# Kernel optimization log

Hardware: AMD Instinct MI355X
Metric: run time of the kernel (lower is better)

Reference implementation:

```python
import jax, jax.numpy as jnp
import numpy as np

N, E, C, D, H = 50000, 1600000, 50000, 128, 512


def setup_inputs() -> dict:
    key = jax.random.key(0)
    ks = jax.random.split(key, 16)
    s = jnp.float32(0.02)  # keep activations stable through 3 layers
    inp = {}
    inp["x"] = jax.random.normal(ks[0], (N, D), jnp.float32)
    inp["edge_index"] = jax.random.randint(ks[1], (2, E), 0, N)
    inp["first_edge"] = jax.random.randint(ks[2], (2,), 0, N)
    inp["candidate_edges"] = jax.random.randint(ks[3], (C, 2), 0, N)
    inp["t"] = jax.random.uniform(ks[4], (1, 1), jnp.float32)
    dims = [(D, H), (H, H), (H, H)]
    i = 5
    for l, (di, do) in enumerate(dims):
        inp[f"gin{l}_w1"] = jax.random.normal(ks[i], (di, do), jnp.float32) * s; i += 1
        inp[f"gin{l}_b1"] = jnp.zeros((do,), jnp.float32)
        inp[f"gin{l}_w2"] = jax.random.normal(ks[i], (do, do), jnp.float32) * s; i += 1
        inp[f"gin{l}_b2"] = jnp.zeros((do,), jnp.float32)
    inp["pred_w1"] = jax.random.normal(ks[i], (5 * H, H), jnp.float32) * s; i += 1
    inp["pred_b1"] = jnp.zeros((H,), jnp.float32)
    inp["pred_w2"] = jax.random.normal(ks[i], (H, 1), jnp.float32) * s; i += 1
    inp["pred_b2"] = jnp.zeros((1,), jnp.float32)
    inp["time_w1"] = jax.random.normal(ks[i], (1, H), jnp.float32) * s; i += 1
    inp["time_b1"] = jnp.zeros((H,), jnp.float32)
    inp["time_w2"] = jax.random.normal(ks[i], (H, H), jnp.float32) * s; i += 1
    inp["time_b2"] = jnp.zeros((H,), jnp.float32)
    return inp


def _edge_rep(x, u, v):
    # 'sum_absdiff': cat([x_u + x_v, |x_u - x_v|]) -> 2*H features
    xu, xv = x[u], x[v]
    return jnp.concatenate([xu + xv, jnp.abs(xu - xv)], axis=-1)


def reference(x, edge_index, first_edge, candidate_edges, t,
              gin0_w1, gin0_b1, gin0_w2, gin0_b2,
              gin1_w1, gin1_b1, gin1_w2, gin1_b2,
              gin2_w1, gin2_b1, gin2_w2, gin2_b2,
              pred_w1, pred_b1, pred_w2, pred_b2,
              time_w1, time_b1, time_w2, time_b2):
    src, dst = edge_index[0], edge_index[1]
    layers = [(gin0_w1, gin0_b1, gin0_w2, gin0_b2),
              (gin1_w1, gin1_b1, gin1_w2, gin1_b2),
              (gin2_w1, gin2_b1, gin2_w2, gin2_b2)]
    # GINConv (eps=0): h_i = MLP(x_i + sum_{j->i} x_j)
    for w1, b1, w2, b2 in layers:
        agg = jax.ops.segment_sum(x[src], dst, num_segments=x.shape[0])
        h = x + agg
        x = jax.nn.relu(h @ w1 + b1) @ w2 + b2
    first_feat = _edge_rep(x, first_edge[0], first_edge[1])  # [2H]
    t_embed = (jax.nn.relu(t @ time_w1 + time_b1) @ time_w2 + time_b2)[0]  # [H]
    cand_feat = _edge_rep(x, candidate_edges[:, 0], candidate_edges[:, 1])  # [C, 2H]
    Cn = cand_feat.shape[0]
    feat = jnp.concatenate([
        jnp.broadcast_to(first_feat, (Cn, first_feat.shape[0])),
        cand_feat,
        jnp.broadcast_to(t_embed, (Cn, t_embed.shape[0])),
    ], axis=-1)  # [C, 5H]
    logits = (jax.nn.relu(feat @ pred_w1 + pred_b1) @ pred_w2 + pred_b2)[:, 0]  # [C]
    return logits
```

## Files before the change

kernel.cpp:

```cpp
#include <hip/hip_runtime.h>

typedef __bf16 bf16x2 __attribute__((ext_vector_type(2)));
typedef __bf16 bf16x4 __attribute__((ext_vector_type(4)));
typedef __bf16 bf16x8 __attribute__((ext_vector_type(8)));
typedef float f32x4 __attribute__((ext_vector_type(4)));

#define LDSTR 40

__global__ void hist_kernel(const int* __restrict__ dst, int* __restrict__ deg, int E) {
    int i = blockIdx.x * 256 + threadIdx.x;
    if (i < E) atomicAdd(&deg[dst[i]], 1);
}

__global__ __launch_bounds__(1024)
void scan_kernel(const int* __restrict__ deg, int* __restrict__ rowptr,
                 int* __restrict__ cursor, int n) {
    __shared__ int part[1024];
    int tid = threadIdx.x;
    int chunk = (n + 1023) >> 10;
    int beg = tid * chunk;
    int fin = min(beg + chunk, n);
    int s = 0;
    for (int i = beg; i < fin; i++) s += deg[i];
    part[tid] = s;
    __syncthreads();
    for (int off = 1; off < 1024; off <<= 1) {
        int v = (tid >= off) ? part[tid - off] : 0;
        __syncthreads();
        part[tid] += v;
        __syncthreads();
    }
    int run = (tid == 0) ? 0 : part[tid - 1];
    for (int i = beg; i < fin; i++) {
        rowptr[i] = run; cursor[i] = run; run += deg[i];
    }
    if (tid == 1023) rowptr[n] = run;
}

__global__ void scatter_kernel(const int* __restrict__ src, const int* __restrict__ dst,
                               int* __restrict__ cursor, int* __restrict__ colsrc, int E) {
    int i = blockIdx.x * 256 + threadIdx.x;
    if (i < E) {
        int p = atomicAdd(&cursor[dst[i]], 1);
        colsrc[p] = src[i];
    }
}

__global__ void f32_to_bf16_kernel(const float* __restrict__ in, __bf16* __restrict__ out, int n4) {
    int i = blockIdx.x * 256 + threadIdx.x;
    if (i < n4) {
        float4 f = ((const float4*)in)[i];
        bf16x4 o;
        o[0] = (__bf16)f.x; o[1] = (__bf16)f.y; o[2] = (__bf16)f.z; o[3] = (__bf16)f.w;
        ((bf16x4*)out)[i] = o;
    }
}

__global__ void wprep_kernel(const float* __restrict__ in, __bf16* __restrict__ out, int kbits) {
    int idx = blockIdx.x * 256 + threadIdx.x;
    int K = 1 << kbits;
    if (idx < (512 << kbits)) {
        int k = idx & (K - 1);
        int n = idx >> kbits;
        out[idx] = (__bf16)in[k * 512 + n];
    }
}

template<int F> struct VecT;
template<> struct VecT<2> { using T = bf16x2; };
template<> struct VecT<8> { using T = bf16x8; };

template<int F, int U>
__global__ __launch_bounds__(256)
void agg_kernel(const __bf16* __restrict__ xb, const int* __restrict__ rowptr,
                const int* __restrict__ colsrc, __bf16* __restrict__ h, int n) {
    const int node = blockIdx.x * 4 + (threadIdx.x >> 6);
    if (node >= n) return;
    const int lane = threadIdx.x & 63;
    const int DIM = F * 64;
    using V = typename VecT<F>::T;

    float acc[F];
    {
        V v = *(const V*)(xb + (size_t)node * DIM + lane * F);
        #pragma unroll
        for (int i = 0; i < F; i++) acc[i] = (float)v[i];
    }

    int e   = __builtin_amdgcn_readfirstlane(rowptr[node]);
    int end = __builtin_amdgcn_readfirstlane(rowptr[node + 1]);
    const __bf16* xl = xb + lane * F;

    for (; e + U <= end; e += U) {
        int s[U];
        #pragma unroll
        for (int j = 0; j < U; j++) s[j] = colsrc[e + j];
        V v[U];
        #pragma unroll
        for (int j = 0; j < U; j++) v[j] = *(const V*)(xl + (size_t)s[j] * DIM);
        #pragma unroll
        for (int j = 0; j < U; j++)
            #pragma unroll
            for (int i = 0; i < F; i++) acc[i] += (float)v[j][i];
    }
    if constexpr (U > 4) {
        for (; e + 4 <= end; e += 4) {
            int s[4];
            #pragma unroll
            for (int j = 0; j < 4; j++) s[j] = colsrc[e + j];
            V v[4];
            #pragma unroll
            for (int j = 0; j < 4; j++) v[j] = *(const V*)(xl + (size_t)s[j] * DIM);
            #pragma unroll
            for (int j = 0; j < 4; j++)
                #pragma unroll
                for (int i = 0; i < F; i++) acc[i] += (float)v[j][i];
        }
    }
    for (; e < end; e++) {
        int s0 = colsrc[e];
        V v = *(const V*)(xl + (size_t)s0 * DIM);
        #pragma unroll
        for (int i = 0; i < F; i++) acc[i] += (float)v[i];
    }

    __bf16* out = h + (size_t)node * DIM + lane * F;
    V o;
    #pragma unroll
    for (int i = 0; i < F; i++) o[i] = (__bf16)acc[i];
    *(V*)out = o;
}

template<int AMODE, bool RELU>
__global__ __launch_bounds__(256, 3)
void gemm_kernel(const __bf16* __restrict__ A, const __bf16* __restrict__ Xb,
                 const int* __restrict__ cand, const __bf16* __restrict__ Bt,
                 const float* __restrict__ bias, __bf16* __restrict__ Cout,
                 int M, int K) {
    __shared__ __bf16 sA[64 * LDSTR];
    __shared__ __bf16 sB[256 * LDSTR];

    const int tid = threadIdx.x;
    const int lane = tid & 63;
    const int waveN = tid >> 6;
    const int mlane = lane & 15;
    const int quad = lane >> 4;
    const int rowBase = blockIdx.x * 64;
    const int nBase = blockIdx.y * 256;

    const int ar = tid >> 2;
    const int ac = (tid & 3) << 3;
    const int br = tid >> 2;
    const int bc = (tid & 3) << 3;

    const f32x4 fzero = {0.f, 0.f, 0.f, 0.f};
    f32x4 acc[4][4];
    #pragma unroll
    for (int i = 0; i < 4; i++)
        #pragma unroll
        for (int j = 0; j < 4; j++) acc[i][j] = fzero;

    int uu = 0, vv = 0;
    const int grow = rowBase + ar;
    if (AMODE == 1 && grow < M) { uu = cand[2 * grow]; vv = cand[2 * grow + 1]; }

    for (int k0 = 0; k0 < K; k0 += 32) {
        __syncthreads();
        {
            bf16x8 av = {};
            if (AMODE == 0) {
                if (grow < M) av = *(const bf16x8*)(A + (size_t)grow * K + k0 + ac);
            } else {
                if (grow < M) {
                    int k = k0 + ac;
                    int kk = k & 511;
                    bf16x8 xu = *(const bf16x8*)(Xb + (size_t)uu * 512 + kk);
                    bf16x8 xv = *(const bf16x8*)(Xb + (size_t)vv * 512 + kk);
                    if (k < 512) {
                        #pragma unroll
                        for (int q = 0; q < 8; q++) av[q] = (__bf16)((float)xu[q] + (float)xv[q]);
                    } else {
                        #pragma unroll
                        for (int q = 0; q < 8; q++) av[q] = (__bf16)fabsf((float)xu[q] - (float)xv[q]);
                    }
                }
            }
            *(bf16x8*)(sA + ar * LDSTR + ac) = av;
        }
        #pragma unroll
        for (int i = 0; i < 4; i++) {
            int nn = br + i * 64;
            bf16x8 b = *(const bf16x8*)(Bt + (size_t)(nBase + nn) * K + k0 + bc);
            *(bf16x8*)(sB + nn * LDSTR + bc) = b;
        }
        __syncthreads();

        bf16x8 aF[4], bF[4];
        #pragma unroll
        for (int mt = 0; mt < 4; mt++)
            aF[mt] = *(const bf16x8*)(sA + (mt * 16 + mlane) * LDSTR + quad * 8);
        #pragma unroll
        for (int nt = 0; nt < 4; nt++)
            bF[nt] = *(const bf16x8*)(sB + (waveN * 64 + nt * 16 + mlane) * LDSTR + quad * 8);
        #pragma unroll
        for (int mt = 0; mt < 4; mt++)
            #pragma unroll
            for (int nt = 0; nt < 4; nt++)
                acc[mt][nt] = __builtin_amdgcn_mfma_f32_16x16x32_bf16(aF[mt], bF[nt], acc[mt][nt], 0, 0, 0);
    }

    #pragma unroll
    for (int mt = 0; mt < 4; mt++) {
        #pragma unroll
        for (int nt = 0; nt < 4; nt++) {
            int col = nBase + waveN * 64 + nt * 16 + mlane;
            float bv = bias[col];
            #pragma unroll
            for (int r = 0; r < 4; r++) {
                int row = rowBase + mt * 16 + quad * 4 + r;
                if (row < M) {
                    float v = acc[mt][nt][r] + bv;
                    if (RELU) v = fmaxf(v, 0.f);
                    Cout[(size_t)row * 512 + col] = (__bf16)v;
                }
            }
        }
    }
}

__global__ __launch_bounds__(512)
void constvec_kernel(const __bf16* __restrict__ xb, const int* __restrict__ first_edge,
                     const float* __restrict__ t,
                     const float* __restrict__ tw1, const float* __restrict__ tb1,
                     const float* __restrict__ tw2, const float* __restrict__ tb2,
                     const float* __restrict__ pw1, const float* __restrict__ pb1,
                     float* __restrict__ cvec) {
    __shared__ float z1[512];
    __shared__ float te[512];
    __shared__ float ff[1024];
    int tid = threadIdx.x;
    float tv = t[0];
    z1[tid] = fmaxf(tv * tw1[tid] + tb1[tid], 0.f);
    int u = first_edge[0], v = first_edge[1];
    float xu = (float)xb[(size_t)u * 512 + tid];
    float xv = (float)xb[(size_t)v * 512 + tid];
    ff[tid] = xu + xv;
    ff[512 + tid] = fabsf(xu - xv);
    __syncthreads();
    float s = tb2[tid];
    for (int j = 0; j < 512; j++) s += z1[j] * tw2[j * 512 + tid];
    te[tid] = s;
    __syncthreads();
    float c = pb1[tid];
    for (int k = 0; k < 1024; k++) c += ff[k] * pw1[k * 512 + tid];
    for (int j = 0; j < 512; j++) c += te[j] * pw1[(2048 + j) * 512 + tid];
    cvec[tid] = c;
}

__global__ __launch_bounds__(256)
void logits_kernel(const __bf16* __restrict__ Z, const float* __restrict__ w2,
                   const float* __restrict__ b2, float* __restrict__ out, int C) {
    int c = blockIdx.x * 4 + (threadIdx.x >> 6);
    if (c >= C) return;
    int lane = threadIdx.x & 63;
    bf16x8 z = *(const bf16x8*)(Z + (size_t)c * 512 + lane * 8);
    const float4* w = (const float4*)(w2 + lane * 8);
    float4 w0 = w[0], w1 = w[1];
    float s = (float)z[0] * w0.x + (float)z[1] * w0.y + (float)z[2] * w0.z + (float)z[3] * w0.w
            + (float)z[4] * w1.x + (float)z[5] * w1.y + (float)z[6] * w1.z + (float)z[7] * w1.w;
    #pragma unroll
    for (int off = 32; off > 0; off >>= 1) s += __shfl_down(s, off);
    if (lane == 0) out[c] = s + b2[0];
}

extern "C" void kernel_launch(void* const* d_in, const int* in_sizes, int n_in,
                              void* d_out, int out_size, void* d_ws, size_t ws_size,
                              hipStream_t stream) {
    (void)n_in; (void)out_size; (void)ws_size;
    const float* x          = (const float*)d_in[0];
    const int*   edge_index = (const int*)d_in[1];
    const int*   first_edge = (const int*)d_in[2];
    const int*   cand       = (const int*)d_in[3];
    const float* t          = (const float*)d_in[4];
    const float* gw1[3] = {(const float*)d_in[5], (const float*)d_in[9],  (const float*)d_in[13]};
    const float* gb1[3] = {(const float*)d_in[6], (const float*)d_in[10], (const float*)d_in[14]};
    const float* gw2[3] = {(const float*)d_in[7], (const float*)d_in[11], (const float*)d_in[15]};
    const float* gb2[3] = {(const float*)d_in[8], (const float*)d_in[12], (const float*)d_in[16]};
    const float* pw1 = (const float*)d_in[17];
    const float* pb1 = (const float*)d_in[18];
    const float* pw2 = (const float*)d_in[19];
    const float* pb2 = (const float*)d_in[20];
    const float* tw1 = (const float*)d_in[21];
    const float* tb1 = (const float*)d_in[22];
    const float* tw2 = (const float*)d_in[23];
    const float* tb2 = (const float*)d_in[24];

    const int N = in_sizes[0] / 128;
    const int E = in_sizes[1] / 2;
    const int C = in_sizes[3] / 2;

    char* p = (char*)d_ws;
    auto alloc = [&](size_t bytes) -> void* {
        void* r = (void*)p;
        p += (bytes + 255) & ~(size_t)255;
        return r;
    };
    __bf16* h    = (__bf16*)alloc((size_t)N * 512 * 2);
    __bf16* u    = (__bf16*)alloc((size_t)N * 512 * 2);
    __bf16* xb   = (__bf16*)alloc((size_t)N * 512 * 2);
    __bf16* wt01 = (__bf16*)alloc((size_t)512 * 128 * 2);
    __bf16* wt02 = (__bf16*)alloc((size_t)512 * 512 * 2);
    __bf16* wt11 = (__bf16*)alloc((size_t)512 * 512 * 2);
    __bf16* wt12 = (__bf16*)alloc((size_t)512 * 512 * 2);
    __bf16* wt21 = (__bf16*)alloc((size_t)512 * 512 * 2);
    __bf16* wt22 = (__bf16*)alloc((size_t)512 * 512 * 2);
    __bf16* wtH  = (__bf16*)alloc((size_t)512 * 1024 * 2);
    int* rowptr = (int*)alloc((size_t)(N + 1) * 4);
    int* deg    = (int*)alloc((size_t)N * 4);
    int* cursor = (int*)alloc((size_t)N * 4);
    int* colsrc = (int*)alloc((size_t)E * 4);
    float* cvec = (float*)alloc(512 * 4);
    __bf16* xb0 = (__bf16*)u;

    const int* src = edge_index;
    const int* dst = edge_index + E;

    hipMemsetAsync(deg, 0, (size_t)N * 4, stream);
    int eb = (E + 255) / 256;
    hist_kernel<<<eb, 256, 0, stream>>>(dst, deg, E);
    scan_kernel<<<1, 1024, 0, stream>>>(deg, rowptr, cursor, N);
    scatter_kernel<<<eb, 256, 0, stream>>>(src, dst, cursor, colsrc, E);

    f32_to_bf16_kernel<<<((N * 128 / 4) + 255) / 256, 256, 0, stream>>>(x, xb0, N * 128 / 4);
    wprep_kernel<<<((512 << 7)  + 255) / 256, 256, 0, stream>>>(gw1[0], wt01, 7);
    wprep_kernel<<<((512 << 9)  + 255) / 256, 256, 0, stream>>>(gw2[0], wt02, 9);
    wprep_kernel<<<((512 << 9)  + 255) / 256, 256, 0, stream>>>(gw1[1], wt11, 9);
    wprep_kernel<<<((512 << 9)  + 255) / 256, 256, 0, stream>>>(gw2[1], wt12, 9);
    wprep_kernel<<<((512 << 9)  + 255) / 256, 256, 0, stream>>>(gw1[2], wt21, 9);
    wprep_kernel<<<((512 << 9)  + 255) / 256, 256, 0, stream>>>(gw2[2], wt22, 9);
    wprep_kernel<<<((512 << 10) + 255) / 256, 256, 0, stream>>>(pw1 + (size_t)1024 * 512, wtH, 10);

    dim3 ggrid((N + 63) / 64, 2);
    int ablocks = (N + 3) / 4;

    agg_kernel<2, 16><<<ablocks, 256, 0, stream>>>(xb0, rowptr, colsrc, h, N);
    gemm_kernel<0, true ><<<ggrid, 256, 0, stream>>>(h, nullptr, nullptr, wt01, gb1[0], u,  N, 128);
    gemm_kernel<0, false><<<ggrid, 256, 0, stream>>>(u, nullptr, nullptr, wt02, gb2[0], xb, N, 512);
    agg_kernel<8, 8><<<ablocks, 256, 0, stream>>>(xb, rowptr, colsrc, h, N);
    gemm_kernel<0, true ><<<ggrid, 256, 0, stream>>>(h, nullptr, nullptr, wt11, gb1[1], u,  N, 512);
    gemm_kernel<0, false><<<ggrid, 256, 0, stream>>>(u, nullptr, nullptr, wt12, gb2[1], xb, N, 512);
    agg_kernel<8, 8><<<ablocks, 256, 0, stream>>>(xb, rowptr, colsrc, h, N);
    gemm_kernel<0, true ><<<ggrid, 256, 0, stream>>>(h, nullptr, nullptr, wt21, gb1[2], u,  N, 512);
    gemm_kernel<0, false><<<ggrid, 256, 0, stream>>>(u, nullptr, nullptr, wt22, gb2[2], xb, N, 512);

    constvec_kernel<<<1, 512, 0, stream>>>(xb, first_edge, t, tw1, tb1, tw2, tb2, pw1, pb1, cvec);
    dim3 hgrid((C + 63) / 64, 2);
    gemm_kernel<1, true><<<hgrid, 256, 0, stream>>>(nullptr, xb, cand, wtH, cvec, u, C, 1024);
    logits_kernel<<<(C + 3) / 4, 256, 0, stream>>>(u, pw2, pb2, (float*)d_out, C);
}
```

Before: 1.464 ms.

## Parallelize CSR prefix scan and split wide aggregation into column halves

Replaces the single-block serial prefix scan over node degrees with a three-kernel scan: per-block sums, a scan of those sums, and a per-block scan. Neighbor aggregation for the 512-wide layers now runs as two passes over 256-column halves with 4-element vectors, so each pass gathers from a smaller working set that is meant to stay cache-resident. The trade-off is that edge indices and row pointers are read twice, and there are extra kernel launches.

```diff
diff --git a/kernel.cpp b/kernel.cpp
--- a/kernel.cpp
+++ b/kernel.cpp
@@ -12,29 +12,57 @@
     if (i < E) atomicAdd(&deg[dst[i]], 1);
 }
 
-__global__ __launch_bounds__(1024)
-void scan_kernel(const int* __restrict__ deg, int* __restrict__ rowptr,
-                 int* __restrict__ cursor, int n) {
-    __shared__ int part[1024];
-    int tid = threadIdx.x;
-    int chunk = (n + 1023) >> 10;
-    int beg = tid * chunk;
-    int fin = min(beg + chunk, n);
-    int s = 0;
-    for (int i = beg; i < fin; i++) s += deg[i];
-    part[tid] = s;
-    __syncthreads();
-    for (int off = 1; off < 1024; off <<= 1) {
-        int v = (tid >= off) ? part[tid - off] : 0;
-        __syncthreads();
-        part[tid] += v;
-        __syncthreads();
-    }
-    int run = (tid == 0) ? 0 : part[tid - 1];
-    for (int i = beg; i < fin; i++) {
-        rowptr[i] = run; cursor[i] = run; run += deg[i];
-    }
-    if (tid == 1023) rowptr[n] = run;
+__global__ __launch_bounds__(256)
+void blocksum_kernel(const int* __restrict__ deg, int* __restrict__ bsum, int n) {
+    __shared__ int red[256];
+    int i = blockIdx.x * 256 + threadIdx.x;
+    red[threadIdx.x] = (i < n) ? deg[i] : 0;
+    __syncthreads();
+    for (int off = 128; off > 0; off >>= 1) {
+        if (threadIdx.x < off) red[threadIdx.x] += red[threadIdx.x + off];
+        __syncthreads();
+    }
+    if (threadIdx.x == 0) bsum[blockIdx.x] = red[0];
+}
+
+__global__ __launch_bounds__(256)
+void scanb_kernel(int* __restrict__ bsum, int nb) {
+    __shared__ int s[256];
+    int t = threadIdx.x;
+    s[t] = (t < nb) ? bsum[t] : 0;
+    __syncthreads();
+    for (int off = 1; off < 256; off <<= 1) {
+        int v = (t >= off) ? s[t - off] : 0;
+        __syncthreads();
+        s[t] += v;
+        __syncthreads();
+    }
+    if (t < nb) bsum[t] = (t == 0) ? 0 : s[t - 1];
+}
+
+__global__ __launch_bounds__(256)
+void scanw_kernel(const int* __restrict__ deg, const int* __restrict__ bsum,
+                  int* __restrict__ rowptr, int* __restrict__ cursor, int n) {
+    __shared__ int s[256];
+    int b = blockIdx.x, t = threadIdx.x;
+    int i = b * 256 + t;
+    int d = (i < n) ? deg[i] : 0;
+    s[t] = d;
+    __syncthreads();
+    for (int off = 1; off < 256; off <<= 1) {
+        int v = (t >= off) ? s[t - off] : 0;
+        __syncthreads();
+        s[t] += v;
+        __syncthreads();
+    }
+    int incl = s[t];
+    int base = bsum[b];
+    if (i < n) {
+        int r = base + incl - d;
+        rowptr[i] = r;
+        cursor[i] = r;
+        if (i == n - 1) rowptr[n] = base + incl;
+    }
 }
 
 __global__ void scatter_kernel(const int* __restrict__ src, const int* __restrict__ dst,
@@ -68,28 +96,29 @@
 
 template<int F> struct VecT;
 template<> struct VecT<2> { using T = bf16x2; };
+template<> struct VecT<4> { using T = bf16x4; };
 template<> struct VecT<8> { using T = bf16x8; };
 
-template<int F, int U>
+template<int F, int U, int STR>
 __global__ __launch_bounds__(256)
 void agg_kernel(const __bf16* __restrict__ xb, const int* __restrict__ rowptr,
-                const int* __restrict__ colsrc, __bf16* __restrict__ h, int n) {
+                const int* __restrict__ colsrc, __bf16* __restrict__ h, int n, int colbase) {
     const int node = blockIdx.x * 4 + (threadIdx.x >> 6);
     if (node >= n) return;
     const int lane = threadIdx.x & 63;
-    const int DIM = F * 64;
     using V = typename VecT<F>::T;
+
+    const __bf16* xl = xb + colbase + lane * F;
 
     float acc[F];
     {
-        V v = *(const V*)(xb + (size_t)node * DIM + lane * F);
+        V v = *(const V*)(xl + (size_t)node * STR);
         #pragma unroll
         for (int i = 0; i < F; i++) acc[i] = (float)v[i];
     }
 
     int e   = __builtin_amdgcn_readfirstlane(rowptr[node]);
     int end = __builtin_amdgcn_readfirstlane(rowptr[node + 1]);
-    const __bf16* xl = xb + lane * F;
 
     for (; e + U <= end; e += U) {
         int s[U];
@@ -97,7 +126,7 @@
         for (int j = 0; j < U; j++) s[j] = colsrc[e + j];
         V v[U];
         #pragma unroll
-        for (int j = 0; j < U; j++) v[j] = *(const V*)(xl + (size_t)s[j] * DIM);
+        for (int j = 0; j < U; j++) v[j] = *(const V*)(xl + (size_t)s[j] * STR);
         #pragma unroll
         for (int j = 0; j < U; j++)
             #pragma unroll
@@ -110,7 +139,7 @@
             for (int j = 0; j < 4; j++) s[j] = colsrc[e + j];
             V v[4];
             #pragma unroll
-            for (int j = 0; j < 4; j++) v[j] = *(const V*)(xl + (size_t)s[j] * DIM);
+            for (int j = 0; j < 4; j++) v[j] = *(const V*)(xl + (size_t)s[j] * STR);
             #pragma unroll
             for (int j = 0; j < 4; j++)
                 #pragma unroll
@@ -119,12 +148,12 @@
     }
     for (; e < end; e++) {
         int s0 = colsrc[e];
-        V v = *(const V*)(xl + (size_t)s0 * DIM);
+        V v = *(const V*)(xl + (size_t)s0 * STR);
         #pragma unroll
         for (int i = 0; i < F; i++) acc[i] += (float)v[i];
     }
 
-    __bf16* out = h + (size_t)node * DIM + lane * F;
+    __bf16* out = h + colbase + (size_t)node * STR + lane * F;
     V o;
     #pragma unroll
     for (int i = 0; i < F; i++) o[i] = (__bf16)acc[i];
@@ -319,6 +348,7 @@
     int* deg    = (int*)alloc((size_t)N * 4);
     int* cursor = (int*)alloc((size_t)N * 4);
     int* colsrc = (int*)alloc((size_t)E * 4);
+    int* bsum   = (int*)alloc((size_t)256 * 4);
     float* cvec = (float*)alloc(512 * 4);
     __bf16* xb0 = (__bf16*)u;
 
@@ -327,8 +357,11 @@
 
     hipMemsetAsync(deg, 0, (size_t)N * 4, stream);
     int eb = (E + 255) / 256;
+    int nb = (N + 255) / 256;
     hist_kernel<<<eb, 256, 0, stream>>>(dst, deg, E);
-    scan_kernel<<<1, 1024, 0, stream>>>(deg, rowptr, cursor, N);
+    blocksum_kernel<<<nb, 256, 0, stream>>>(deg, bsum, N);
+    scanb_kernel<<<1, 256, 0, stream>>>(bsum, nb);
+    scanw_kernel<<<nb, 256, 0, stream>>>(deg, bsum, rowptr, cursor, N);
     scatter_kernel<<<eb, 256, 0, stream>>>(src, dst, cursor, colsrc, E);
 
     f32_to_bf16_kernel<<<((N * 128 / 4) + 255) / 256, 256, 0, stream>>>(x, xb0, N * 128 / 4);
@@ -343,13 +376,15 @@
     dim3 ggrid((N + 63) / 64, 2);
     int ablocks = (N + 3) / 4;
 
-    agg_kernel<2, 16><<<ablocks, 256, 0, stream>>>(xb0, rowptr, colsrc, h, N);
+    agg_kernel<2, 16, 128><<<ablocks, 256, 0, stream>>>(xb0, rowptr, colsrc, h, N, 0);
     gemm_kernel<0, true ><<<ggrid, 256, 0, stream>>>(h, nullptr, nullptr, wt01, gb1[0], u,  N, 128);
     gemm_kernel<0, false><<<ggrid, 256, 0, stream>>>(u, nullptr, nullptr, wt02, gb2[0], xb, N, 512);
-    agg_kernel<8, 8><<<ablocks, 256, 0, stream>>>(xb, rowptr, colsrc, h, N);
+    agg_kernel<4, 8, 512><<<ablocks, 256, 0, stream>>>(xb, rowptr, colsrc, h, N, 0);
+    agg_kernel<4, 8, 512><<<ablocks, 256, 0, stream>>>(xb, rowptr, colsrc, h, N, 256);
     gemm_kernel<0, true ><<<ggrid, 256, 0, stream>>>(h, nullptr, nullptr, wt11, gb1[1], u,  N, 512);
     gemm_kernel<0, false><<<ggrid, 256, 0, stream>>>(u, nullptr, nullptr, wt12, gb2[1], xb, N, 512);
-    agg_kernel<8, 8><<<ablocks, 256, 0, stream>>>(xb, rowptr, colsrc, h, N);
+    agg_kernel<4, 8, 512><<<ablocks, 256, 0, stream>>>(xb, rowptr, colsrc, h, N, 0);
+    agg_kernel<4, 8, 512><<<ablocks, 256, 0, stream>>>(xb, rowptr, colsrc, h, N, 256);
     gemm_kernel<0, true ><<<ggrid, 256, 0, stream>>>(h, nullptr, nullptr, wt21, gb1[2], u,  N, 512);
     gemm_kernel<0, false><<<ggrid, 256, 0, stream>>>(u, nullptr, nullptr, wt22, gb2[2], xb, N, 512);
 
```

Result: faster. 1.300 ms (-11.2%).
